# Optimization experiments

Hardware: AMD Instinct MI355X
Metric: run time of the kernel (lower is better)

Reference implementation:

```python
import jax, jax.numpy as jnp
import numpy as np

D_MODEL = 1024
NHEAD = 16
HEAD_DIM = D_MODEL // NHEAD


def setup_inputs() -> dict:
    key = jax.random.key(0)
    ks = jax.random.split(key, 11)
    B, S = 4, 2048
    s = 1.0 / np.sqrt(D_MODEL)
    return {
        "q": jax.random.normal(ks[0], (B, S, D_MODEL), jnp.float32),
        "k": jax.random.normal(ks[1], (B, S, D_MODEL), jnp.float32),
        "v": jax.random.normal(ks[2], (B, S, D_MODEL), jnp.float32),
        "Wq": jax.random.normal(ks[3], (D_MODEL, D_MODEL), jnp.float32) * s,
        "bq": jnp.zeros((D_MODEL,), jnp.float32),
        "Wk": jax.random.normal(ks[4], (D_MODEL, D_MODEL), jnp.float32) * s,
        "bk": jnp.zeros((D_MODEL,), jnp.float32),
        "Wv": jax.random.normal(ks[5], (D_MODEL, D_MODEL), jnp.float32) * s,
        "bv": jnp.zeros((D_MODEL,), jnp.float32),
        "Wo": jax.random.normal(ks[6], (D_MODEL, D_MODEL), jnp.float32) * s,
        "bo": jnp.zeros((D_MODEL,), jnp.float32),
    }


def reference(q, k, v, Wq, bq, Wk, bk, Wv, bv, Wo, bo):
    B, S, _ = q.shape
    H, Dh = NHEAD, HEAD_DIM

    def proj(x, W, b):  # nn.Linear: x @ W.T + b, then split heads -> [B,H,S,Dh]
        y = x @ W.T + b
        return y.reshape(B, S, H, Dh).transpose(0, 2, 1, 3)

    qh = proj(q, Wq, bq)
    kh = proj(k, Wk, bk)
    vh = proj(v, Wv, bv)

    scores = jnp.einsum("bhsd,bhtd->bhst", qh, kh) / jnp.sqrt(jnp.float32(Dh))
    attn = jax.nn.softmax(scores, axis=-1)
    out = jnp.einsum("bhst,bhtd->bhsd", attn, vh)  # [B,H,S,Dh]
    out = out.transpose(0, 2, 1, 3).reshape(B, S, H * Dh)
    return out @ Wo.T + bo
```

## Files before the change

### kernel.cpp

```cpp
#include <hip/hip_runtime.h>


typedef short bf16x8 __attribute__((ext_vector_type(8)));
typedef short bf16x4 __attribute__((ext_vector_type(4)));
typedef float f32x4 __attribute__((ext_vector_type(4)));
typedef float f32x16 __attribute__((ext_vector_type(16)));
typedef unsigned int u32x4 __attribute__((ext_vector_type(4)));

__device__ __forceinline__ short f2bf(float x) {
    union { float f; unsigned int u; } un; un.f = x;
    unsigned int u = un.u;
    return (short)(unsigned short)((u + 0x7fffu + ((u >> 16) & 1u)) >> 16);
}

__device__ __forceinline__ void gll16(const void* g, void* l) {
    __builtin_amdgcn_global_load_lds(
        (const __attribute__((address_space(1))) void*)g,
        (__attribute__((address_space(3))) void*)l, 16, 0, 0);
}

__device__ __forceinline__ void plswap(unsigned& a, unsigned& b) {
    asm("v_permlane32_swap_b32 %0, %1" : "+v"(a), "+v"(b));
}

struct CvtArgs { const float* s[4]; unsigned short* d[4]; int n4; };
__global__ __launch_bounds__(256) void cvt_bf16(CvtArgs ca) {
    const float* s = ca.s[blockIdx.y];
    unsigned short* d = ca.d[blockIdx.y];
    int i = blockIdx.x * blockDim.x + threadIdx.x;
    int stride = gridDim.x * blockDim.x;
    const float4* s4 = reinterpret_cast<const float4*>(s);
    bf16x4* d4 = reinterpret_cast<bf16x4*>(d);
    for (; i < ca.n4; i += stride) {
        float4 x = s4[i];
        bf16x4 y;
        y[0] = f2bf(x.x); y[1] = f2bf(x.y); y[2] = f2bf(x.z); y[3] = f2bf(x.w);
        d4[i] = y;
    }
}

__device__ __forceinline__ void gemm_core(const unsigned short* __restrict__ A,
                                          const unsigned short* __restrict__ W,
                                          const float* __restrict__ bias,
                                          float scale, void* __restrict__ out,
                                          int mode) {
    __shared__ unsigned short As[128 * 64];
    __shared__ unsigned short Bs[128 * 64];
    const int tid = threadIdx.x;
    const int m0 = blockIdx.y * 128, n0 = blockIdx.x * 128;
    const int wave = tid >> 6, lane = tid & 63;
    const int wm = (wave >> 1) * 64, wn = (wave & 1) * 64;
    const int l15 = lane & 15, quad = lane >> 4;
    const int srow = tid >> 3;
    const int scol = ((tid & 7) ^ (srow & 7)) * 8;
    const int cb = (l15 & 7);

    f32x4 acc[4][4] = {};

    for (int k0 = 0; k0 < 1024; k0 += 64) {
        __syncthreads();
#pragma unroll
        for (int ro = 0; ro < 4; ++ro) {
            gll16(&A[(size_t)(m0 + ro * 32 + srow) * 1024 + k0 + scol], &As[ro * 2048 + tid * 8]);
            gll16(&W[(size_t)(n0 + ro * 32 + srow) * 1024 + k0 + scol], &Bs[ro * 2048 + tid * 8]);
        }
        __syncthreads();
#pragma unroll
        for (int kk = 0; kk < 2; ++kk) {
            const int co = ((4 * kk + quad) ^ cb) * 8;
            bf16x8 a[4], b[4];
#pragma unroll
            for (int i = 0; i < 4; ++i)
                a[i] = *reinterpret_cast<bf16x8*>(&As[(wm + i * 16 + l15) * 64 + co]);
#pragma unroll
            for (int j = 0; j < 4; ++j)
                b[j] = *reinterpret_cast<bf16x8*>(&Bs[(wn + j * 16 + l15) * 64 + co]);
#pragma unroll
            for (int i = 0; i < 4; ++i)
#pragma unroll
                for (int j = 0; j < 4; ++j)
                    acc[i][j] = __builtin_amdgcn_mfma_f32_16x16x32_bf16(a[i], b[j], acc[i][j], 0, 0, 0);
        }
    }

#pragma unroll
    for (int i = 0; i < 4; ++i) {
#pragma unroll
        for (int j = 0; j < 4; ++j) {
#pragma unroll
            for (int r = 0; r < 4; ++r) {
                int m = m0 + wm + i * 16 + quad * 4 + r;
                int n = n0 + wn + j * 16 + l15;
                float val = (acc[i][j][r] + bias[n]) * scale;
                if (mode == 0) {
                    reinterpret_cast<float*>(out)[(size_t)m * 1024 + n] = val;
                } else {
                    int b_ = m >> 11, s = m & 2047, h = n >> 6, d = n & 63;
                    size_t off = (mode == 1)
                                     ? ((size_t)((b_ * 16 + h) * 2048 + s) * 64 + d)
                                     : ((size_t)((b_ * 16 + h) * 64 + d) * 2048 + s);
                    reinterpret_cast<unsigned short*>(out)[off] = (unsigned short)f2bf(val);
                }
            }
        }
    }
}

struct QkvArgs {
    const unsigned short* A[3];
    const unsigned short* W[3];
    const float* bias[3];
    float scale[3];
    unsigned short* out[3];
    int mode[3];
};
__global__ __launch_bounds__(256) void gemm_qkv(QkvArgs ga) {
    int z = blockIdx.z;
    gemm_core(ga.A[z], ga.W[z], ga.bias[z], ga.scale[z], ga.out[z], ga.mode[z]);
}

__global__ __launch_bounds__(256) void gemm_wo(const unsigned short* __restrict__ A,
                                               const unsigned short* __restrict__ W,
                                               const float* __restrict__ bias,
                                               float* __restrict__ out) {
    gemm_core(A, W, bias, 1.0f, out, 0);
}

__global__ __launch_bounds__(256, 3) void flash_attn(const unsigned short* __restrict__ Qh,
                                                     const unsigned short* __restrict__ Kh,
                                                     const unsigned short* __restrict__ Vt,
                                                     unsigned short* __restrict__ Oa) {
    __shared__ unsigned short Ks[2][64 * 64];
    __shared__ unsigned short Vs[2][64 * 64];
    const int tid = threadIdx.x;
    const int bh = blockIdx.y;
    const int q0 = blockIdx.x * 128;
    const unsigned short* Qb = Qh + (size_t)bh * 2048 * 64;
    const unsigned short* Kb = Kh + (size_t)bh * 2048 * 64;
    const unsigned short* Vb = Vt + (size_t)bh * 64 * 2048;
    const int wave = tid >> 6, lane = tid & 63;
    const int l31 = lane & 31, hi = lane >> 5;
    const int wq = wave * 32;
    const int srow = tid >> 3;
    const int scol = ((tid & 7) ^ (srow & 7)) * 8;

    int chx[4], rowoff[2];
#pragma unroll
    for (int c = 0; c < 4; ++c) chx[c] = ((c * 2 + hi) ^ (l31 & 7)) * 8;
    rowoff[0] = l31 * 64;
    rowoff[1] = (32 + l31) * 64;

    bf16x8 qreg[4];
#pragma unroll
    for (int c = 0; c < 4; ++c)
        qreg[c] = *reinterpret_cast<const bf16x8*>(
            &Qb[(size_t)(q0 + wq + l31) * 64 + c * 16 + hi * 8]);

    f32x16 o[2] = {};
    float lacc = 0.f;

#pragma unroll
    for (int ro = 0; ro < 2; ++ro) {
        gll16(&Kb[(size_t)(ro * 32 + srow) * 64 + scol], &Ks[0][ro * 2048 + tid * 8]);
        gll16(&Vb[(size_t)(ro * 32 + srow) * 2048 + scol], &Vs[0][ro * 2048 + tid * 8]);
    }
    __syncthreads();

    for (int it = 0; it < 32; ++it) {
        const int buf = it & 1;
        if (it < 31) {
            int kvn = (it + 1) * 64;
#pragma unroll
            for (int ro = 0; ro < 2; ++ro) {
                gll16(&Kb[(size_t)(kvn + ro * 32 + srow) * 64 + scol], &Ks[buf ^ 1][ro * 2048 + tid * 8]);
                gll16(&Vb[(size_t)(ro * 32 + srow) * 2048 + kvn + scol], &Vs[buf ^ 1][ro * 2048 + tid * 8]);
            }
        }

        f32x16 sacc[2] = {};
#pragma unroll
        for (int c = 0; c < 4; ++c) {
            bf16x8 ak0 = *reinterpret_cast<bf16x8*>(&Ks[buf][rowoff[0] + chx[c]]);
            bf16x8 ak1 = *reinterpret_cast<bf16x8*>(&Ks[buf][rowoff[1] + chx[c]]);
            sacc[0] = __builtin_amdgcn_mfma_f32_32x32x16_bf16(ak0, qreg[c], sacc[0], 0, 0, 0);
            sacc[1] = __builtin_amdgcn_mfma_f32_32x32x16_bf16(ak1, qreg[c], sacc[1], 0, 0, 0);
        }

        bf16x8 pa[4];
#pragma unroll
        for (int mt = 0; mt < 2; ++mt) {
            float e[16];
#pragma unroll
            for (int r = 0; r < 16; ++r) e[r] = __builtin_amdgcn_exp2f(sacc[mt][r]);
            float s01 = (e[0] + e[1]) + (e[2] + e[3]);
            float s23 = (e[4] + e[5]) + (e[6] + e[7]);
            float s45 = (e[8] + e[9]) + (e[10] + e[11]);
            float s67 = (e[12] + e[13]) + (e[14] + e[15]);
            lacc += (s01 + s23) + (s45 + s67);
            unsigned w[8];
#pragma unroll
            for (int t = 0; t < 8; ++t) {
                union { float f; unsigned u; } a0{e[2 * t]}, a1{e[2 * t + 1]};
                w[t] = __builtin_amdgcn_perm(a1.u + 0x8000u, a0.u + 0x8000u, 0x07060302u);
            }
            plswap(w[0], w[2]); plswap(w[1], w[3]);
            plswap(w[4], w[6]); plswap(w[5], w[7]);
            u32x4 t0; t0[0] = w[0]; t0[1] = w[1]; t0[2] = w[2]; t0[3] = w[3];
            u32x4 t1; t1[0] = w[4]; t1[1] = w[5]; t1[2] = w[6]; t1[3] = w[7];
            pa[mt * 2 + 0] = __builtin_bit_cast(bf16x8, t0);
            pa[mt * 2 + 1] = __builtin_bit_cast(bf16x8, t1);
        }

#pragma unroll
        for (int cg = 0; cg < 4; ++cg) {
#pragma unroll
            for (int nt = 0; nt < 2; ++nt) {
                bf16x8 bv = *reinterpret_cast<bf16x8*>(&Vs[buf][rowoff[nt] + chx[cg]]);
                o[nt] = __builtin_amdgcn_mfma_f32_32x32x16_bf16(pa[cg], bv, o[nt], 0, 0, 0);
            }
        }
        __syncthreads();
    }

    float lfull = lacc + __shfl_xor(lacc, 32, 64);
    float rinv = 1.0f / lfull;
    const int b_ = bh >> 4, h = bh & 15;
#pragma unroll
    for (int r = 0; r < 16; ++r) {
        const int qrow = (r & 3) + 8 * (r >> 2) + 4 * hi;
        const float rl = __shfl(rinv, qrow, 64);
        const int s = q0 + wq + qrow;
#pragma unroll
        for (int nt = 0; nt < 2; ++nt) {
            const int d = nt * 32 + l31;
            Oa[(size_t)(b_ * 2048 + s) * 1024 + h * 64 + d] =
                (unsigned short)f2bf(o[nt][r] * rl);
        }
    }
}

extern "C" void kernel_launch(void* const* d_in, const int* in_sizes, int n_in,
                              void* d_out, int out_size, void* d_ws, size_t ws_size,
                              hipStream_t stream) {
    const float* q  = (const float*)d_in[0];
    const float* k  = (const float*)d_in[1];
    const float* v  = (const float*)d_in[2];
    const float* Wq = (const float*)d_in[3];
    const float* bq = (const float*)d_in[4];
    const float* Wk = (const float*)d_in[5];
    const float* bk = (const float*)d_in[6];
    const float* Wv = (const float*)d_in[7];
    const float* bv = (const float*)d_in[8];
    const float* Wo = (const float*)d_in[9];
    const float* bo = (const float*)d_in[10];

    const size_t E = (size_t)8192 * 1024;
    const size_t WE = (size_t)1024 * 1024;
    unsigned short* r0 = (unsigned short*)d_ws;
    unsigned short* r1 = r0 + E;
    unsigned short* r2 = r1 + E;
    unsigned short* r3 = r2 + E;
    unsigned short* wqb = r3 + E;
    unsigned short* wkb = wqb + WE;
    unsigned short* wvb = wkb + WE;
    unsigned short* wob = wvb + WE;

    CvtArgs ca;
    ca.s[0] = q; ca.d[0] = r0;
    ca.s[1] = k; ca.d[1] = r1;
    ca.s[2] = v; ca.d[2] = r2;
    ca.s[3] = q; ca.d[3] = r0;
    ca.n4 = (int)(E / 4);
    cvt_bf16<<<dim3(1024, 3), 256, 0, stream>>>(ca);

    CvtArgs cw;
    cw.s[0] = Wq; cw.d[0] = wqb;
    cw.s[1] = Wk; cw.d[1] = wkb;
    cw.s[2] = Wv; cw.d[2] = wvb;
    cw.s[3] = Wo; cw.d[3] = wob;
    cw.n4 = (int)(WE / 4);
    cvt_bf16<<<dim3(256, 4), 256, 0, stream>>>(cw);

    const float QSCALE = 0.125f * 1.44269504088896340736f;

    QkvArgs ga;
    ga.A[0] = r0; ga.W[0] = wqb; ga.bias[0] = bq; ga.scale[0] = QSCALE; ga.out[0] = r3; ga.mode[0] = 1;
    ga.A[1] = r1; ga.W[1] = wkb; ga.bias[1] = bk; ga.scale[1] = 1.0f;   ga.out[1] = r0; ga.mode[1] = 1;
    ga.A[2] = r2; ga.W[2] = wvb; ga.bias[2] = bv; ga.scale[2] = 1.0f;   ga.out[2] = r1; ga.mode[2] = 2;
    gemm_qkv<<<dim3(8, 64, 3), 256, 0, stream>>>(ga);

    flash_attn<<<dim3(16, 64), 256, 0, stream>>>(r3, r0, r1, r2);
    gemm_wo<<<dim3(8, 64), 256, 0, stream>>>(r2, wob, bo, (float*)d_out);
}
```

Measured before the change: 377.4 us.

## Software-pipeline QK and softmax-PV in flash attention, transpose V projection GEMM

After: 384.2 us. No clear change (+1.8%).

```diff
diff --git a/kernel.cpp b/kernel.cpp
--- a/kernel.cpp
+++ b/kernel.cpp
@@ -47,7 +47,8 @@
     __shared__ unsigned short As[128 * 64];
     __shared__ unsigned short Bs[128 * 64];
     const int tid = threadIdx.x;
-    const int m0 = blockIdx.y * 128, n0 = blockIdx.x * 128;
+    const int m0 = (mode == 2 ? blockIdx.x : blockIdx.y) * 128;
+    const int n0 = (mode == 2 ? blockIdx.y : blockIdx.x) * 128;
     const int wave = tid >> 6, lane = tid & 63;
     const int wm = (wave >> 1) * 64, wn = (wave & 1) * 64;
     const int l15 = lane & 15, quad = lane >> 4;
@@ -91,14 +92,16 @@
             for (int r = 0; r < 4; ++r) {
                 int m = m0 + wm + i * 16 + quad * 4 + r;
                 int n = n0 + wn + j * 16 + l15;
-                float val = (acc[i][j][r] + bias[n]) * scale;
+                float val = (acc[i][j][r] + bias[mode == 2 ? m : n]) * scale;
                 if (mode == 0) {
                     reinterpret_cast<float*>(out)[(size_t)m * 1024 + n] = val;
+                } else if (mode == 1) {
+                    int b_ = m >> 11, s = m & 2047, h = n >> 6, d = n & 63;
+                    size_t off = (size_t)((b_ * 16 + h) * 2048 + s) * 64 + d;
+                    reinterpret_cast<unsigned short*>(out)[off] = (unsigned short)f2bf(val);
                 } else {
-                    int b_ = m >> 11, s = m & 2047, h = n >> 6, d = n & 63;
-                    size_t off = (mode == 1)
-                                     ? ((size_t)((b_ * 16 + h) * 2048 + s) * 64 + d)
-                                     : ((size_t)((b_ * 16 + h) * 64 + d) * 2048 + s);
+                    int h = m >> 6, d = m & 63, b_ = n >> 11, s = n & 2047;
+                    size_t off = (size_t)((b_ * 16 + h) * 64 + d) * 2048 + s;
                     reinterpret_cast<unsigned short*>(out)[off] = (unsigned short)f2bf(val);
                 }
             }
@@ -126,7 +129,53 @@
     gemm_core(A, W, bias, 1.0f, out, 0);
 }
 
-__global__ __launch_bounds__(256, 3) void flash_attn(const unsigned short* __restrict__ Qh,
+
+#define SOFTMAX_PV(MT, VBASE)                                                        \
+    {                                                                                \
+        float e[16];                                                                 \
+        _Pragma("unroll")                                                            \
+        for (int r = 0; r < 16; ++r) e[r] = __builtin_amdgcn_exp2f(sacc[MT][r]);     \
+        lacc += ((e[0] + e[1]) + (e[2] + e[3])) + ((e[4] + e[5]) + (e[6] + e[7])) +  \
+                ((e[8] + e[9]) + (e[10] + e[11])) + ((e[12] + e[13]) + (e[14] + e[15])); \
+        unsigned w[8];                                                               \
+        _Pragma("unroll")                                                            \
+        for (int t = 0; t < 8; ++t) {                                                \
+            union { float f; unsigned u; } a0{e[2 * t]}, a1{e[2 * t + 1]};           \
+            w[t] = __builtin_amdgcn_perm(a1.u + 0x8000u, a0.u + 0x8000u, 0x07060302u); \
+        }                                                                            \
+        plswap(w[0], w[2]); plswap(w[1], w[3]);                                      \
+        plswap(w[4], w[6]); plswap(w[5], w[7]);                                      \
+        u32x4 t0; t0[0] = w[0]; t0[1] = w[1]; t0[2] = w[2]; t0[3] = w[3];            \
+        u32x4 t1; t1[0] = w[4]; t1[1] = w[5]; t1[2] = w[6]; t1[3] = w[7];            \
+        bf16x8 pa0 = __builtin_bit_cast(bf16x8, t0);                                 \
+        bf16x8 pa1 = __builtin_bit_cast(bf16x8, t1);                                 \
+        __builtin_amdgcn_s_setprio(1);                                               \
+        _Pragma("unroll")                                                            \
+        for (int nt = 0; nt < 2; ++nt) {                                             \
+            bf16x8 bv0 = *reinterpret_cast<const bf16x8*>(&(VBASE)[rowoff[nt] + chx[2 * (MT)]]); \
+            bf16x8 bv1 = *reinterpret_cast<const bf16x8*>(&(VBASE)[rowoff[nt] + chx[2 * (MT) + 1]]); \
+            o[nt] = __builtin_amdgcn_mfma_f32_32x32x16_bf16(pa0, bv0, o[nt], 0, 0, 0); \
+            o[nt] = __builtin_amdgcn_mfma_f32_32x32x16_bf16(pa1, bv1, o[nt], 0, 0, 0); \
+        }                                                                            \
+        __builtin_amdgcn_s_setprio(0);                                               \
+    }
+
+#define QK_TILE(KBASE)                                                               \
+    {                                                                                \
+        f32x16 zz = {};                                                              \
+        sacc[0] = zz; sacc[1] = zz;                                                  \
+        __builtin_amdgcn_s_setprio(1);                                               \
+        _Pragma("unroll")                                                            \
+        for (int c = 0; c < 4; ++c) {                                                \
+            bf16x8 ak0 = *reinterpret_cast<const bf16x8*>(&(KBASE)[rowoff[0] + chx[c]]); \
+            bf16x8 ak1 = *reinterpret_cast<const bf16x8*>(&(KBASE)[rowoff[1] + chx[c]]); \
+            sacc[0] = __builtin_amdgcn_mfma_f32_32x32x16_bf16(ak0, qreg[c], sacc[0], 0, 0, 0); \
+            sacc[1] = __builtin_amdgcn_mfma_f32_32x32x16_bf16(ak1, qreg[c], sacc[1], 0, 0, 0); \
+        }                                                                            \
+        __builtin_amdgcn_s_setprio(0);                                               \
+    }
+
+__global__ __launch_bounds__(256, 4) void flash_attn(const unsigned short* __restrict__ Qh,
                                                      const unsigned short* __restrict__ Kh,
                                                      const unsigned short* __restrict__ Vt,
                                                      unsigned short* __restrict__ Oa) {
@@ -157,70 +206,43 @@
             &Qb[(size_t)(q0 + wq + l31) * 64 + c * 16 + hi * 8]);
 
     f32x16 o[2] = {};
+    f32x16 sacc[2];
     float lacc = 0.f;
 
 #pragma unroll
     for (int ro = 0; ro < 2; ++ro) {
         gll16(&Kb[(size_t)(ro * 32 + srow) * 64 + scol], &Ks[0][ro * 2048 + tid * 8]);
         gll16(&Vb[(size_t)(ro * 32 + srow) * 2048 + scol], &Vs[0][ro * 2048 + tid * 8]);
+        gll16(&Kb[(size_t)(64 + ro * 32 + srow) * 64 + scol], &Ks[1][ro * 2048 + tid * 8]);
     }
     __syncthreads();
-
-    for (int it = 0; it < 32; ++it) {
-        const int buf = it & 1;
-        if (it < 31) {
-            int kvn = (it + 1) * 64;
-#pragma unroll
-            for (int ro = 0; ro < 2; ++ro) {
-                gll16(&Kb[(size_t)(kvn + ro * 32 + srow) * 64 + scol], &Ks[buf ^ 1][ro * 2048 + tid * 8]);
-                gll16(&Vb[(size_t)(ro * 32 + srow) * 2048 + kvn + scol], &Vs[buf ^ 1][ro * 2048 + tid * 8]);
-            }
-        }
-
-        f32x16 sacc[2] = {};
-#pragma unroll
-        for (int c = 0; c < 4; ++c) {
-            bf16x8 ak0 = *reinterpret_cast<bf16x8*>(&Ks[buf][rowoff[0] + chx[c]]);
-            bf16x8 ak1 = *reinterpret_cast<bf16x8*>(&Ks[buf][rowoff[1] + chx[c]]);
-            sacc[0] = __builtin_amdgcn_mfma_f32_32x32x16_bf16(ak0, qreg[c], sacc[0], 0, 0, 0);
-            sacc[1] = __builtin_amdgcn_mfma_f32_32x32x16_bf16(ak1, qreg[c], sacc[1], 0, 0, 0);
-        }
-
-        bf16x8 pa[4];
-#pragma unroll
-        for (int mt = 0; mt < 2; ++mt) {
-            float e[16];
-#pragma unroll
-            for (int r = 0; r < 16; ++r) e[r] = __builtin_amdgcn_exp2f(sacc[mt][r]);
-            float s01 = (e[0] + e[1]) + (e[2] + e[3]);
-            float s23 = (e[4] + e[5]) + (e[6] + e[7]);
-            float s45 = (e[8] + e[9]) + (e[10] + e[11]);
-            float s67 = (e[12] + e[13]) + (e[14] + e[15]);
-            lacc += (s01 + s23) + (s45 + s67);
-            unsigned w[8];
-#pragma unroll
-            for (int t = 0; t < 8; ++t) {
-                union { float f; unsigned u; } a0{e[2 * t]}, a1{e[2 * t + 1]};
-                w[t] = __builtin_amdgcn_perm(a1.u + 0x8000u, a0.u + 0x8000u, 0x07060302u);
-            }
-            plswap(w[0], w[2]); plswap(w[1], w[3]);
-            plswap(w[4], w[6]); plswap(w[5], w[7]);
-            u32x4 t0; t0[0] = w[0]; t0[1] = w[1]; t0[2] = w[2]; t0[3] = w[3];
-            u32x4 t1; t1[0] = w[4]; t1[1] = w[5]; t1[2] = w[6]; t1[3] = w[7];
-            pa[mt * 2 + 0] = __builtin_bit_cast(bf16x8, t0);
-            pa[mt * 2 + 1] = __builtin_bit_cast(bf16x8, t1);
-        }
-
-#pragma unroll
-        for (int cg = 0; cg < 4; ++cg) {
-#pragma unroll
-            for (int nt = 0; nt < 2; ++nt) {
-                bf16x8 bv = *reinterpret_cast<bf16x8*>(&Vs[buf][rowoff[nt] + chx[cg]]);
-                o[nt] = __builtin_amdgcn_mfma_f32_32x32x16_bf16(pa[cg], bv, o[nt], 0, 0, 0);
-            }
-        }
+    QK_TILE(Ks[0]);
+    __syncthreads();
+
+    for (int it = 0; it < 31; ++it) {
+        const int cur = it & 1, nxt = cur ^ 1;
+        if (it < 30) {
+            const int kvn = (it + 2) * 64;
+#pragma unroll
+            for (int ro = 0; ro < 2; ++ro)
+                gll16(&Kb[(size_t)(kvn + ro * 32 + srow) * 64 + scol], &Ks[cur][ro * 2048 + tid * 8]);
+        }
+        {
+            const int kvn = (it + 1) * 64;
+#pragma unroll
+            for (int ro = 0; ro < 2; ++ro)
+                gll16(&Vb[(size_t)(ro * 32 + srow) * 2048 + kvn + scol], &Vs[nxt][ro * 2048 + tid * 8]);
+        }
+
+        SOFTMAX_PV(0, Vs[cur]);
+        SOFTMAX_PV(1, Vs[cur]);
+
+        QK_TILE(Ks[nxt]);
+
         __syncthreads();
     }
+    SOFTMAX_PV(0, Vs[1]);
+    SOFTMAX_PV(1, Vs[1]);
 
     float lfull = lacc + __shfl_xor(lacc, 32, 64);
     float rinv = 1.0f / lfull;
@@ -284,9 +306,9 @@
     const float QSCALE = 0.125f * 1.44269504088896340736f;
 
     QkvArgs ga;
-    ga.A[0] = r0; ga.W[0] = wqb; ga.bias[0] = bq; ga.scale[0] = QSCALE; ga.out[0] = r3; ga.mode[0] = 1;
-    ga.A[1] = r1; ga.W[1] = wkb; ga.bias[1] = bk; ga.scale[1] = 1.0f;   ga.out[1] = r0; ga.mode[1] = 1;
-    ga.A[2] = r2; ga.W[2] = wvb; ga.bias[2] = bv; ga.scale[2] = 1.0f;   ga.out[2] = r1; ga.mode[2] = 2;
+    ga.A[0] = r0;  ga.W[0] = wqb; ga.bias[0] = bq; ga.scale[0] = QSCALE; ga.out[0] = r3; ga.mode[0] = 1;
+    ga.A[1] = r1;  ga.W[1] = wkb; ga.bias[1] = bk; ga.scale[1] = 1.0f;   ga.out[1] = r0; ga.mode[1] = 1;
+    ga.A[2] = wvb; ga.W[2] = r2;  ga.bias[2] = bv; ga.scale[2] = 1.0f;   ga.out[2] = r1; ga.mode[2] = 2;
     gemm_qkv<<<dim3(8, 64, 3), 256, 0, stream>>>(ga);
 
     flash_attn<<<dim3(16, 64), 256, 0, stream>>>(r3, r0, r1, r2);
```
